# Performance work log

Hardware: AMD Instinct MI355X
Metric: run time of the kernel (lower is better)

The kernel has to match this reference:

```python
import jax, jax.numpy as jnp
import numpy as np

B, N, E, H = 16, 577, 1024, 16          # batch, tokens (1 cls + 24x24 patches), embed, heads
HD = E // H
LORA_E, LORA_R = 4, 16                   # LoRA experts, rank
AD_E, AD_D = 4, 64                       # adapter experts, bottleneck
FF = 4 * E


def setup_inputs() -> dict:
    key = jax.random.key(0)
    ks = jax.random.split(key, 12)
    p = lambda i, shape: jax.random.normal(ks[i], shape, dtype=jnp.float32) * 0.02
    return {
        "tokens": jax.random.normal(ks[0], (B, N, E), dtype=jnp.float32),
        "ln1_g": jnp.ones((E,), jnp.float32), "ln1_b": jnp.zeros((E,), jnp.float32),
        "qkv_w": p(1, (3 * E, E)), "qkv_b": jnp.zeros((3 * E,), jnp.float32),
        "proj_w": p(2, (E, E)), "proj_b": jnp.zeros((E,), jnp.float32),
        "lora_gate_w": p(3, (LORA_E, E)),
        "lora_A": p(4, (LORA_E, LORA_R, E)),
        "lora_B": p(5, (LORA_E, 3 * E, LORA_R)),
        "ln2_g": jnp.ones((E,), jnp.float32), "ln2_b": jnp.zeros((E,), jnp.float32),
        "fc1_w": p(6, (FF, E)), "fc1_b": jnp.zeros((FF,), jnp.float32),
        "fc2_w": p(7, (E, FF)), "fc2_b": jnp.zeros((E,), jnp.float32),
        "ad_gate_w": p(8, (AD_E, E)),
        "ad_down_w": p(9, (AD_E, AD_D, E)), "ad_down_b": jnp.zeros((AD_E, AD_D), jnp.float32),
        "ad_up_w": p(10, (AD_E, E, AD_D)), "ad_up_b": jnp.zeros((AD_E, E), jnp.float32),
    }


def _ln(x, g, b):
    m = x.mean(-1, keepdims=True)
    v = ((x - m) ** 2).mean(-1, keepdims=True)
    return (x - m) * jax.lax.rsqrt(v + 1e-6) * g + b


def reference(tokens, ln1_g, ln1_b, qkv_w, qkv_b, proj_w, proj_b,
              lora_gate_w, lora_A, lora_B, ln2_g, ln2_b,
              fc1_w, fc1_b, fc2_w, fc2_b,
              ad_gate_w, ad_down_w, ad_down_b, ad_up_w, ad_up_b):
    # ---- attention with MoE-LoRA delta on fused QKV ----
    normed = _ln(tokens, ln1_g, ln1_b)                      # [B,N,E]
    qkv = normed @ qkv_w.T + qkv_b                          # [B,N,3E]
    gates = jax.nn.softmax(normed @ lora_gate_w.T, axis=-1)  # [B,N,X]
    h = jnp.einsum('bnd,xrd->bnxr', normed, lora_A)         # low-rank down
    delta = jnp.einsum('bnxr,bnx,xor->bno', h, gates, lora_B)  # gate-weighted up
    qkv = (qkv + delta).reshape(B, N, 3, H, HD).transpose(2, 0, 3, 1, 4)
    q, k, v = qkv[0], qkv[1], qkv[2]                        # [B,H,N,hd]
    scores = jnp.einsum('bhqd,bhkd->bhqk', q, k) * (HD ** -0.5)
    probs = jax.nn.softmax(scores, axis=-1)
    ctx = jnp.einsum('bhqk,bhkd->bhqd', probs, v)
    ctx = ctx.transpose(0, 2, 1, 3).reshape(B, N, E)
    tokens = tokens + (ctx @ proj_w.T + proj_b)
    # ---- MLP + MoE adapter branch (shared norm2 input) ----
    mlp_in = _ln(tokens, ln2_g, ln2_b)
    mlp_out = jax.nn.gelu(mlp_in @ fc1_w.T + fc1_b, approximate=False) @ fc2_w.T + fc2_b
    ag = jax.nn.softmax(mlp_in @ ad_gate_w.T, axis=-1)       # [B,N,Xa]
    ah = jax.nn.gelu(jnp.einsum('bnd,xhd->bnxh', mlp_in, ad_down_w) + ad_down_b,
                     approximate=False)
    ad_out = (jnp.einsum('bnxh,bnx,xoh->bno', ah, ag, ad_up_w)
              + jnp.einsum('bnx,xo->bno', ag, ad_up_b))
    return tokens + mlp_out + ad_out
```

## Files before the change

### kernel.cpp

```cpp
#include <hip/hip_runtime.h>
#include <math.h>

#define TOK 9232
#define EMB 1024
#define NQKV 3072
#define FFD 4096
#define NSEQ 577

typedef __bf16 bf16x8 __attribute__((ext_vector_type(8)));
typedef float f32x4 __attribute__((ext_vector_type(4)));
typedef unsigned short ushort8 __attribute__((ext_vector_type(8)));
typedef unsigned short ushort4v __attribute__((ext_vector_type(4)));

typedef __attribute__((address_space(3))) unsigned int lds_u32_t;
typedef const __attribute__((address_space(1))) unsigned int glob_u32_t;

__device__ __forceinline__ void async16(void* lds, const void* g) {
    __builtin_amdgcn_global_load_lds((glob_u32_t*)g, (lds_u32_t*)lds, 16, 0, 0);
}

__device__ __forceinline__ unsigned short f2bf(float f) {
    unsigned int u = __builtin_bit_cast(unsigned int, f);
    u = (u + 0x7fffu + ((u >> 16) & 1u)) >> 16;
    return (unsigned short)u;
}
__device__ __forceinline__ float bf2f(unsigned short s) {
    unsigned int u = ((unsigned int)s) << 16;
    return __builtin_bit_cast(float, u);
}
__device__ __forceinline__ float gelu_exact(float x) {
    return 0.5f * x * (1.0f + erff(x * 0.70710678118654752f));
}

__global__ void k_f32_to_bf16(const float* __restrict__ in, unsigned short* __restrict__ out, int n) {
    int i = blockIdx.x * 256 + threadIdx.x;
    if (i < n) out[i] = f2bf(in[i]);
}
__global__ void k_pack_bcat(const float* __restrict__ Bw, unsigned short* __restrict__ out) {
    int i = blockIdx.x * 256 + threadIdx.x;
    if (i >= 4 * 3072 * 16) return;
    int x = i / (3072 * 16);
    int rem = i - x * (3072 * 16);
    int o = rem >> 4;
    int r = rem & 15;
    out[o * 64 + x * 16 + r] = f2bf(Bw[i]);
}
__global__ void k_pack_u(const float* __restrict__ Uw, unsigned short* __restrict__ out) {
    int i = blockIdx.x * 256 + threadIdx.x;
    if (i >= 4 * 1024 * 64) return;
    int x = i >> 16;
    int o = (i >> 6) & 1023;
    int h = i & 63;
    out[o * 256 + x * 64 + h] = f2bf(Uw[i]);
}

__global__ __launch_bounds__(256) void k_ln_gates(const float* __restrict__ x,
                                                  const float* __restrict__ g,
                                                  const float* __restrict__ b,
                                                  const float* __restrict__ gw,
                                                  unsigned short* __restrict__ out,
                                                  float* __restrict__ gates) {
    int t = blockIdx.x;
    int tid = threadIdx.x;
    const float* xp = x + (size_t)t * EMB;
    float4 v = ((const float4*)xp)[tid];
    float s = v.x + v.y + v.z + v.w;
    float sq = v.x * v.x + v.y * v.y + v.z * v.z + v.w * v.w;
    #pragma unroll
    for (int off = 32; off > 0; off >>= 1) {
        s += __shfl_down(s, off);
        sq += __shfl_down(sq, off);
    }
    __shared__ float red[8];
    if ((tid & 63) == 0) { red[tid >> 6] = s; red[(tid >> 6) + 4] = sq; }
    __syncthreads();
    float S = red[0] + red[1] + red[2] + red[3];
    float SQ = red[4] + red[5] + red[6] + red[7];
    float mean = S * (1.0f / EMB);
    float var = SQ * (1.0f / EMB) - mean * mean;
    float rstd = rsqrtf(var + 1e-6f);
    float4 gv = ((const float4*)g)[tid];
    float4 bv = ((const float4*)b)[tid];
    float n0 = (v.x - mean) * rstd * gv.x + bv.x;
    float n1 = (v.y - mean) * rstd * gv.y + bv.y;
    float n2 = (v.z - mean) * rstd * gv.z + bv.z;
    float n3 = (v.w - mean) * rstd * gv.w + bv.w;
    ushort4v o;
    o[0] = f2bf(n0); o[1] = f2bf(n1); o[2] = f2bf(n2); o[3] = f2bf(n3);
    ((ushort4v*)(out + (size_t)t * EMB))[tid] = o;
    float p[4];
    #pragma unroll
    for (int xx = 0; xx < 4; ++xx) {
        float4 gr = ((const float4*)(gw + xx * EMB))[tid];
        p[xx] = n0 * gr.x + n1 * gr.y + n2 * gr.z + n3 * gr.w;
    }
    #pragma unroll
    for (int off = 32; off > 0; off >>= 1) {
        #pragma unroll
        for (int xx = 0; xx < 4; ++xx) p[xx] += __shfl_down(p[xx], off);
    }
    __shared__ float red2[4][4];
    if ((tid & 63) == 0) {
        #pragma unroll
        for (int xx = 0; xx < 4; ++xx) red2[tid >> 6][xx] = p[xx];
    }
    __syncthreads();
    if (tid == 0) {
        float l[4];
        #pragma unroll
        for (int xx = 0; xx < 4; ++xx) l[xx] = red2[0][xx] + red2[1][xx] + red2[2][xx] + red2[3][xx];
        float m = fmaxf(fmaxf(l[0], l[1]), fmaxf(l[2], l[3]));
        float e[4], ssum = 0.f;
        #pragma unroll
        for (int xx = 0; xx < 4; ++xx) { e[xx] = expf(l[xx] - m); ssum += e[xx]; }
        float inv = 1.0f / ssum;
        #pragma unroll
        for (int xx = 0; xx < 4; ++xx) gates[t * 4 + xx] = e[xx] * inv;
    }
}

__global__ void k_make_hw(const float* __restrict__ gates, const float* __restrict__ lh,
                          unsigned short* __restrict__ hw) {
    int i = blockIdx.x * 256 + threadIdx.x;
    if (i >= TOK * 64) return;
    int t = i >> 6;
    int j = i & 63;
    hw[i] = f2bf(gates[t * 4 + (j >> 4)] * lh[i]);
}

__global__ void k_make_ahw(const float* __restrict__ ag, const float* __restrict__ ahpre,
                           unsigned short* __restrict__ ahw) {
    int i = blockIdx.x * 256 + threadIdx.x;
    if (i >= TOK * 256) return;
    int t = i >> 8;
    int j = i & 255;
    ahw[i] = f2bf(ag[t * 4 + (j >> 6)] * gelu_exact(ahpre[i]));
}

__global__ __launch_bounds__(256) void k_adbias(const float* __restrict__ ag,
                                                const float* __restrict__ upb,
                                                float* __restrict__ tok2) {
    int t = blockIdx.x;
    int tid = threadIdx.x;
    float g0 = ag[t * 4 + 0], g1 = ag[t * 4 + 1], g2 = ag[t * 4 + 2], g3 = ag[t * 4 + 3];
    float4 b0 = ((const float4*)(upb + 0 * EMB))[tid];
    float4 b1 = ((const float4*)(upb + 1 * EMB))[tid];
    float4 b2 = ((const float4*)(upb + 2 * EMB))[tid];
    float4 b3 = ((const float4*)(upb + 3 * EMB))[tid];
    float4 r = ((float4*)(tok2 + (size_t)t * EMB))[tid];
    r.x += g0 * b0.x + g1 * b1.x + g2 * b2.x + g3 * b3.x;
    r.y += g0 * b0.y + g1 * b1.y + g2 * b2.y + g3 * b3.y;
    r.z += g0 * b0.z + g1 * b1.z + g2 * b2.z + g3 * b3.z;
    r.w += g0 * b0.w + g1 * b1.w + g2 * b2.w + g3 * b3.w;
    ((float4*)(tok2 + (size_t)t * EMB))[tid] = r;
}

template<bool GELU, bool BF16OUT>
__global__ __launch_bounds__(256) void k_gemm(
    const unsigned short* __restrict__ A, const unsigned short* __restrict__ W,
    int M, int N, int K,
    const unsigned short* __restrict__ A2, const unsigned short* __restrict__ W2, int K2,
    const float* __restrict__ bias, const float* __restrict__ resid,
    void* __restrict__ Cout, int ldc, int gy)
{
    __shared__ unsigned short As[128][32];
    __shared__ unsigned short Ws[128][32];
    int tid = threadIdx.x;

    int nwg = gridDim.x;
    int orig = blockIdx.x;
    int xcd = orig & 7, lid = orig >> 3;
    int q = nwg >> 3, r = nwg & 7;
    int wg = (xcd < r ? xcd * (q + 1) : r * (q + 1) + (xcd - r) * q) + lid;
    int bm128 = (wg / gy) * 128;
    int bn128 = (wg % gy) * 128;

    int l = tid & 63, w = tid >> 6;
    int wr = w >> 1, wc = w & 1;
    int lr = l & 15, lk = (l >> 4) * 8;
    int srow = l >> 2;
    int sslot = (l & 3) * 8;

    f32x4 acc[4][4];
    #pragma unroll
    for (int m = 0; m < 4; ++m)
        #pragma unroll
        for (int n = 0; n < 4; ++n) acc[m][n] = (f32x4){0.f, 0.f, 0.f, 0.f};

    auto kloop = [&](const unsigned short* __restrict__ Ap,
                     const unsigned short* __restrict__ Wp, int Kc) {
        for (int k0 = 0; k0 < Kc; k0 += 32) {
            #pragma unroll
            for (int i = 0; i < 2; ++i) {
                int row = w * 32 + i * 16 + srow;
                int ra = bm128 + row; if (ra >= M) ra = M - 1;
                async16((char*)&As[0][0] + w * 2048 + i * 1024,
                        Ap + (size_t)ra * Kc + k0 + sslot);
                int rb = bn128 + row; if (rb >= N) rb = N - 1;
                async16((char*)&Ws[0][0] + w * 2048 + i * 1024,
                        Wp + (size_t)rb * Kc + k0 + sslot);
            }
            __syncthreads();
            bf16x8 af[4], bfr[4];
            #pragma unroll
            for (int m = 0; m < 4; ++m) af[m] = *(const bf16x8*)&As[wr * 64 + m * 16 + lr][lk];
            #pragma unroll
            for (int n = 0; n < 4; ++n) bfr[n] = *(const bf16x8*)&Ws[wc * 64 + n * 16 + lr][lk];
            #pragma unroll
            for (int m = 0; m < 4; ++m)
                #pragma unroll
                for (int n = 0; n < 4; ++n)
                    acc[m][n] = __builtin_amdgcn_mfma_f32_16x16x32_bf16(af[m], bfr[n], acc[m][n], 0, 0, 0);
            __syncthreads();
        }
    };
    kloop(A, W, K);
    if (A2) kloop(A2, W2, K2);

    int rb0 = bm128 + wr * 64;
    int cb0 = bn128 + wc * 64;
    #pragma unroll
    for (int n = 0; n < 4; ++n) {
        int col = cb0 + n * 16 + lr;
        if (col >= N) continue;
        float bv = bias ? bias[col] : 0.0f;
        #pragma unroll
        for (int m = 0; m < 4; ++m) {
            #pragma unroll
            for (int rr = 0; rr < 4; ++rr) {
                int row = rb0 + m * 16 + (l >> 4) * 4 + rr;
                if (row >= M) continue;
                float c = acc[m][n][rr] + bv;
                if (GELU) c = gelu_exact(c);
                if (resid) c += resid[(size_t)row * ldc + col];
                if (BF16OUT) ((unsigned short*)Cout)[(size_t)row * ldc + col] = f2bf(c);
                else ((float*)Cout)[(size_t)row * ldc + col] = c;
            }
        }
    }
}

__global__ __launch_bounds__(256) void k_attn(const unsigned short* __restrict__ qkv,
                                              unsigned short* __restrict__ ctx) {
    int bh = blockIdx.x;
    int qt = blockIdx.y;
    int b = bh >> 4, h = bh & 15;
    int tid = threadIdx.x;
    int l = tid & 63;
    int w = tid >> 6;
    int lr = l & 15;
    int lk = (l >> 4) * 8;

    __shared__ unsigned short Qs[64][72];
    __shared__ unsigned short Ks[64][72];
    __shared__ unsigned short Vt[64][72];
    __shared__ unsigned short Ps[64][72];

    const size_t base = (size_t)b * NSEQ * NQKV + (size_t)h * 64;
    int q0 = qt * 64;

    {
        int row = tid >> 2, ds = (tid & 3) * 16;
        int qrow = q0 + row;
        if (qrow < NSEQ) {
            const unsigned short* src = qkv + base + (size_t)qrow * NQKV + ds;
            #pragma unroll
            for (int j = 0; j < 16; ++j) Qs[row][ds + j] = f2bf(bf2f(src[j]) * 0.125f);
        } else {
            #pragma unroll
            for (int j = 0; j < 16; ++j) Qs[row][ds + j] = 0;
        }
    }

    float m_run[4], l_run[4];
    f32x4 o[4];
    #pragma unroll
    for (int r = 0; r < 4; ++r) { m_run[r] = -1e30f; l_run[r] = 0.0f; }
    #pragma unroll
    for (int n = 0; n < 4; ++n) o[n] = (f32x4){0.f, 0.f, 0.f, 0.f};

    for (int kt = 0; kt < 10; ++kt) {
        __syncthreads();
        {
            int row = tid >> 2, ds = (tid & 3) * 16;
            int key = kt * 64 + row;
            if (key < NSEQ) {
                const unsigned short* ksrc = qkv + base + (size_t)key * NQKV + 1024 + ds;
                *(ushort8*)&Ks[row][ds] = *(const ushort8*)ksrc;
                *(ushort8*)&Ks[row][ds + 8] = *(const ushort8*)(ksrc + 8);
                const unsigned short* vsrc = qkv + base + (size_t)key * NQKV + 2048 + ds;
                #pragma unroll
                for (int j = 0; j < 16; ++j) Vt[ds + j][row] = vsrc[j];
            } else {
                ushort8 z = {};
                *(ushort8*)&Ks[row][ds] = z;
                *(ushort8*)&Ks[row][ds + 8] = z;
                #pragma unroll
                for (int j = 0; j < 16; ++j) Vt[ds + j][row] = 0;
            }
        }
        __syncthreads();

        f32x4 s[4];
        #pragma unroll
        for (int n = 0; n < 4; ++n) s[n] = (f32x4){0.f, 0.f, 0.f, 0.f};
        #pragma unroll
        for (int ks = 0; ks < 2; ++ks) {
            bf16x8 qa = *(const bf16x8*)&Qs[w * 16 + lr][ks * 32 + lk];
            #pragma unroll
            for (int n = 0; n < 4; ++n) {
                bf16x8 kb = *(const bf16x8*)&Ks[n * 16 + lr][ks * 32 + lk];
                s[n] = __builtin_amdgcn_mfma_f32_16x16x32_bf16(qa, kb, s[n], 0, 0, 0);
            }
        }
        #pragma unroll
        for (int n = 0; n < 4; ++n) {
            int col = kt * 64 + n * 16 + lr;
            if (col >= NSEQ) {
                #pragma unroll
                for (int r = 0; r < 4; ++r) s[n][r] = -1e30f;
            }
        }
        float tmax[4];
        #pragma unroll
        for (int r = 0; r < 4; ++r)
            tmax[r] = fmaxf(fmaxf(s[0][r], s[1][r]), fmaxf(s[2][r], s[3][r]));
        #pragma unroll
        for (int off = 1; off < 16; off <<= 1) {
            #pragma unroll
            for (int r = 0; r < 4; ++r) tmax[r] = fmaxf(tmax[r], __shfl_xor(tmax[r], off));
        }
        float alpha[4], rs[4];
        #pragma unroll
        for (int r = 0; r < 4; ++r) {
            float mn = fmaxf(m_run[r], tmax[r]);
            alpha[r] = __expf(m_run[r] - mn);
            m_run[r] = mn;
            rs[r] = 0.0f;
        }
        #pragma unroll
        for (int n = 0; n < 4; ++n) {
            #pragma unroll
            for (int r = 0; r < 4; ++r) {
                float p = __expf(s[n][r] - m_run[r]);
                s[n][r] = p;
                rs[r] += p;
            }
        }
        #pragma unroll
        for (int off = 1; off < 16; off <<= 1) {
            #pragma unroll
            for (int r = 0; r < 4; ++r) rs[r] += __shfl_xor(rs[r], off);
        }
        #pragma unroll
        for (int r = 0; r < 4; ++r) l_run[r] = l_run[r] * alpha[r] + rs[r];
        #pragma unroll
        for (int n = 0; n < 4; ++n) {
            #pragma unroll
            for (int r = 0; r < 4; ++r) o[n][r] *= alpha[r];
        }
        #pragma unroll
        for (int n = 0; n < 4; ++n) {
            #pragma unroll
            for (int r = 0; r < 4; ++r)
                Ps[w * 16 + (l >> 4) * 4 + r][n * 16 + lr] = f2bf(s[n][r]);
        }
        __syncthreads();
        #pragma unroll
        for (int ks = 0; ks < 2; ++ks) {
            bf16x8 pa = *(const bf16x8*)&Ps[w * 16 + lr][ks * 32 + lk];
            #pragma unroll
            for (int n = 0; n < 4; ++n) {
                bf16x8 vb = *(const bf16x8*)&Vt[n * 16 + lr][ks * 32 + lk];
                o[n] = __builtin_amdgcn_mfma_f32_16x16x32_bf16(pa, vb, o[n], 0, 0, 0);
            }
        }
    }
    #pragma unroll
    for (int r = 0; r < 4; ++r) {
        int qrow = q0 + w * 16 + (l >> 4) * 4 + r;
        if (qrow < NSEQ) {
            float inv = (l_run[r] > 0.f) ? 1.0f / l_run[r] : 0.0f;
            #pragma unroll
            for (int n = 0; n < 4; ++n)
                ctx[((size_t)b * NSEQ + qrow) * EMB + h * 64 + n * 16 + lr] = f2bf(o[n][r] * inv);
        }
    }
}

extern "C" void kernel_launch(void* const* d_in, const int* in_sizes, int n_in,
                              void* d_out, int out_size, void* d_ws, size_t ws_size,
                              hipStream_t stream) {
    const float* tokens      = (const float*)d_in[0];
    const float* ln1_g       = (const float*)d_in[1];
    const float* ln1_b       = (const float*)d_in[2];
    const float* qkv_w       = (const float*)d_in[3];
    const float* qkv_b       = (const float*)d_in[4];
    const float* proj_w      = (const float*)d_in[5];
    const float* proj_b      = (const float*)d_in[6];
    const float* lora_gate_w = (const float*)d_in[7];
    const float* lora_A      = (const float*)d_in[8];
    const float* lora_B      = (const float*)d_in[9];
    const float* ln2_g       = (const float*)d_in[10];
    const float* ln2_b       = (const float*)d_in[11];
    const float* fc1_w       = (const float*)d_in[12];
    const float* fc1_b       = (const float*)d_in[13];
    const float* fc2_w       = (const float*)d_in[14];
    const float* fc2_b       = (const float*)d_in[15];
    const float* ad_gate_w   = (const float*)d_in[16];
    const float* ad_down_w   = (const float*)d_in[17];
    const float* ad_down_b   = (const float*)d_in[18];
    const float* ad_up_w     = (const float*)d_in[19];
    const float* ad_up_b     = (const float*)d_in[20];

    char* ws = (char*)d_ws;
    size_t off = 0;
    auto alloc = [&](size_t bytes) -> void* {
        void* p = ws + off;
        off += (bytes + 255) & ~(size_t)255;
        return p;
    };

    unsigned short* w_qkv  = (unsigned short*)alloc((size_t)NQKV * EMB * 2);
    unsigned short* w_proj = (unsigned short*)alloc((size_t)EMB * EMB * 2);
    unsigned short* w_fc1  = (unsigned short*)alloc((size_t)FFD * EMB * 2);
    unsigned short* w_fc2  = (unsigned short*)alloc((size_t)EMB * FFD * 2);
    unsigned short* w_acat = (unsigned short*)alloc((size_t)64 * EMB * 2);
    unsigned short* w_bcat = (unsigned short*)alloc((size_t)NQKV * 64 * 2);
    unsigned short* w_dcat = (unsigned short*)alloc((size_t)256 * EMB * 2);
    unsigned short* w_u    = (unsigned short*)alloc((size_t)EMB * 256 * 2);

    unsigned short* u1 = (unsigned short*)alloc((size_t)TOK * EMB * 2);
    char*           u2 = (char*)alloc((size_t)TOK * EMB * 2);
    unsigned short* u3 = (unsigned short*)alloc((size_t)TOK * FFD * 2);
    float* tok2   = (float*)alloc((size_t)TOK * EMB * 4);
    float* lora_h = (float*)alloc((size_t)TOK * 64 * 4);
    unsigned short* hw = (unsigned short*)alloc((size_t)TOK * 64 * 2);
    float* gates = (float*)alloc((size_t)TOK * 4 * 4);
    float* ag    = (float*)alloc((size_t)TOK * 4 * 4);

    unsigned short* normed = u1;
    unsigned short* mlpin  = u1;
    unsigned short* ctx    = (unsigned short*)u2;
    float*          ahpre  = (float*)u2;
    unsigned short* ahw    = (unsigned short*)(u2 + (size_t)TOK * 256 * 4);
    unsigned short* qkv    = u3;
    unsigned short* h1     = u3;

    k_f32_to_bf16<<<(NQKV * EMB + 255) / 256, 256, 0, stream>>>(qkv_w, w_qkv, NQKV * EMB);
    k_f32_to_bf16<<<(EMB * EMB + 255) / 256, 256, 0, stream>>>(proj_w, w_proj, EMB * EMB);
    k_f32_to_bf16<<<(FFD * EMB + 255) / 256, 256, 0, stream>>>(fc1_w, w_fc1, FFD * EMB);
    k_f32_to_bf16<<<(EMB * FFD + 255) / 256, 256, 0, stream>>>(fc2_w, w_fc2, EMB * FFD);
    k_f32_to_bf16<<<(64 * EMB + 255) / 256, 256, 0, stream>>>(lora_A, w_acat, 64 * EMB);
    k_pack_bcat<<<(NQKV * 64 + 255) / 256, 256, 0, stream>>>(lora_B, w_bcat);
    k_f32_to_bf16<<<(256 * EMB + 255) / 256, 256, 0, stream>>>(ad_down_w, w_dcat, 256 * EMB);
    k_pack_u<<<(EMB * 256 + 255) / 256, 256, 0, stream>>>(ad_up_w, w_u);

    k_ln_gates<<<TOK, 256, 0, stream>>>(tokens, ln1_g, ln1_b, lora_gate_w, normed, gates);
    k_gemm<false, false><<<73 * 1, 256, 0, stream>>>(
        normed, w_acat, TOK, 64, EMB, nullptr, nullptr, 0, nullptr, nullptr, lora_h, 64, 1);
    k_make_hw<<<(TOK * 64 + 255) / 256, 256, 0, stream>>>(gates, lora_h, hw);
    k_gemm<false, true><<<73 * 24, 256, 0, stream>>>(
        normed, w_qkv, TOK, NQKV, EMB, hw, w_bcat, 64, qkv_b, nullptr, qkv, NQKV, 24);
    k_attn<<<dim3(256, 10), 256, 0, stream>>>(qkv, ctx);
    k_gemm<false, false><<<73 * 8, 256, 0, stream>>>(
        ctx, w_proj, TOK, EMB, EMB, nullptr, nullptr, 0, proj_b, tokens, tok2, EMB, 8);
    k_ln_gates<<<TOK, 256, 0, stream>>>(tok2, ln2_g, ln2_b, ad_gate_w, mlpin, ag);
    k_gemm<false, false><<<73 * 2, 256, 0, stream>>>(
        mlpin, w_dcat, TOK, 256, EMB, nullptr, nullptr, 0, ad_down_b, nullptr, ahpre, 256, 2);
    k_make_ahw<<<(TOK * 256 + 255) / 256, 256, 0, stream>>>(ag, ahpre, ahw);
    k_adbias<<<TOK, 256, 0, stream>>>(ag, ad_up_b, tok2);
    k_gemm<true, true><<<73 * 32, 256, 0, stream>>>(
        mlpin, w_fc1, TOK, FFD, EMB, nullptr, nullptr, 0, fc1_b, nullptr, h1, FFD, 32);
    k_gemm<false, false><<<73 * 8, 256, 0, stream>>>(
        h1, w_fc2, TOK, EMB, FFD, ahw, w_u, 256, fc2_b, tok2, d_out, EMB, 8);
}
```

Measured before the change: 785.6 us.

## Fuse gating into GEMM epilogues, split-K fc2 with atomics, batch weight packing

```diff
diff --git a/kernel.cpp b/kernel.cpp
--- a/kernel.cpp
+++ b/kernel.cpp
@@ -32,26 +32,38 @@
     return 0.5f * x * (1.0f + erff(x * 0.70710678118654752f));
 }
 
-__global__ void k_f32_to_bf16(const float* __restrict__ in, unsigned short* __restrict__ out, int n) {
-    int i = blockIdx.x * 256 + threadIdx.x;
-    if (i < n) out[i] = f2bf(in[i]);
+__global__ void k_pack_all(const float* __restrict__ s_qkv, const float* __restrict__ s_proj,
+                           const float* __restrict__ s_fc1, const float* __restrict__ s_fc2,
+                           const float* __restrict__ s_la,  const float* __restrict__ s_ad,
+                           unsigned short* __restrict__ d_qkv, unsigned short* __restrict__ d_proj,
+                           unsigned short* __restrict__ d_fc1, unsigned short* __restrict__ d_fc2,
+                           unsigned short* __restrict__ d_la,  unsigned short* __restrict__ d_ad) {
+    int stride = gridDim.x * 256;
+    for (int i4 = blockIdx.x * 256 + threadIdx.x; i4 < 3227648; i4 += stride) {
+        const float* s; unsigned short* d; int local;
+        if (i4 < 786432)       { s = s_qkv;  d = d_qkv;  local = i4; }
+        else if (i4 < 1048576) { s = s_proj; d = d_proj; local = i4 - 786432; }
+        else if (i4 < 2097152) { s = s_fc1;  d = d_fc1;  local = i4 - 1048576; }
+        else if (i4 < 3145728) { s = s_fc2;  d = d_fc2;  local = i4 - 2097152; }
+        else if (i4 < 3162112) { s = s_la;   d = d_la;   local = i4 - 3145728; }
+        else                   { s = s_ad;   d = d_ad;   local = i4 - 3162112; }
+        float4 v = ((const float4*)s)[local];
+        ushort4v o;
+        o[0] = f2bf(v.x); o[1] = f2bf(v.y); o[2] = f2bf(v.z); o[3] = f2bf(v.w);
+        ((ushort4v*)d)[local] = o;
+    }
 }
 __global__ void k_pack_bcat(const float* __restrict__ Bw, unsigned short* __restrict__ out) {
     int i = blockIdx.x * 256 + threadIdx.x;
-    if (i >= 4 * 3072 * 16) return;
-    int x = i / (3072 * 16);
-    int rem = i - x * (3072 * 16);
-    int o = rem >> 4;
-    int r = rem & 15;
-    out[o * 64 + x * 16 + r] = f2bf(Bw[i]);
+    if (i >= 3072 * 64) return;
+    int o = i >> 6, j = i & 63, x = j >> 4, r = j & 15;
+    out[o * 64 + j] = f2bf(Bw[x * 3072 * 16 + o * 16 + r]);
 }
 __global__ void k_pack_u(const float* __restrict__ Uw, unsigned short* __restrict__ out) {
     int i = blockIdx.x * 256 + threadIdx.x;
-    if (i >= 4 * 1024 * 64) return;
-    int x = i >> 16;
-    int o = (i >> 6) & 1023;
-    int h = i & 63;
-    out[o * 256 + x * 64 + h] = f2bf(Uw[i]);
+    if (i >= 1024 * 256) return;
+    int o = i >> 8, j = i & 255, x = j >> 6, h = j & 63;
+    out[o * 256 + j] = f2bf(Uw[x * 65536 + o * 64 + h]);
 }
 
 __global__ __launch_bounds__(256) void k_ln_gates(const float* __restrict__ x,
@@ -119,27 +131,11 @@
     }
 }
 
-__global__ void k_make_hw(const float* __restrict__ gates, const float* __restrict__ lh,
-                          unsigned short* __restrict__ hw) {
-    int i = blockIdx.x * 256 + threadIdx.x;
-    if (i >= TOK * 64) return;
-    int t = i >> 6;
-    int j = i & 63;
-    hw[i] = f2bf(gates[t * 4 + (j >> 4)] * lh[i]);
-}
-
-__global__ void k_make_ahw(const float* __restrict__ ag, const float* __restrict__ ahpre,
-                           unsigned short* __restrict__ ahw) {
-    int i = blockIdx.x * 256 + threadIdx.x;
-    if (i >= TOK * 256) return;
-    int t = i >> 8;
-    int j = i & 255;
-    ahw[i] = f2bf(ag[t * 4 + (j >> 6)] * gelu_exact(ahpre[i]));
-}
-
-__global__ __launch_bounds__(256) void k_adbias(const float* __restrict__ ag,
-                                                const float* __restrict__ upb,
-                                                float* __restrict__ tok2) {
+__global__ __launch_bounds__(256) void k_fc2init(const float* __restrict__ tok2,
+                                                 const float* __restrict__ fc2b,
+                                                 const float* __restrict__ ag,
+                                                 const float* __restrict__ upb,
+                                                 float* __restrict__ out) {
     int t = blockIdx.x;
     int tid = threadIdx.x;
     float g0 = ag[t * 4 + 0], g1 = ag[t * 4 + 1], g2 = ag[t * 4 + 2], g3 = ag[t * 4 + 3];
@@ -147,33 +143,37 @@
     float4 b1 = ((const float4*)(upb + 1 * EMB))[tid];
     float4 b2 = ((const float4*)(upb + 2 * EMB))[tid];
     float4 b3 = ((const float4*)(upb + 3 * EMB))[tid];
-    float4 r = ((float4*)(tok2 + (size_t)t * EMB))[tid];
-    r.x += g0 * b0.x + g1 * b1.x + g2 * b2.x + g3 * b3.x;
-    r.y += g0 * b0.y + g1 * b1.y + g2 * b2.y + g3 * b3.y;
-    r.z += g0 * b0.z + g1 * b1.z + g2 * b2.z + g3 * b3.z;
-    r.w += g0 * b0.w + g1 * b1.w + g2 * b2.w + g3 * b3.w;
-    ((float4*)(tok2 + (size_t)t * EMB))[tid] = r;
-}
-
-template<bool GELU, bool BF16OUT>
+    float4 fb = ((const float4*)fc2b)[tid];
+    float4 r = ((const float4*)(tok2 + (size_t)t * EMB))[tid];
+    r.x += fb.x + g0 * b0.x + g1 * b1.x + g2 * b2.x + g3 * b3.x;
+    r.y += fb.y + g0 * b0.y + g1 * b1.y + g2 * b2.y + g3 * b3.y;
+    r.z += fb.z + g0 * b0.z + g1 * b1.z + g2 * b2.z + g3 * b3.z;
+    r.w += fb.w + g0 * b0.w + g1 * b1.w + g2 * b2.w + g3 * b3.w;
+    ((float4*)(out + (size_t)t * EMB))[tid] = r;
+}
+
+template<bool GELU, bool BF16OUT, bool ATOMIC, int GG, int KS>
 __global__ __launch_bounds__(256) void k_gemm(
-    const unsigned short* __restrict__ A, const unsigned short* __restrict__ W,
-    int M, int N, int K,
+    const unsigned short* __restrict__ A, int lda,
+    const unsigned short* __restrict__ W, int ldw, int klen,
+    int M, int N,
     const unsigned short* __restrict__ A2, const unsigned short* __restrict__ W2, int K2,
     const float* __restrict__ bias, const float* __restrict__ resid,
+    const float* __restrict__ aux,
     void* __restrict__ Cout, int ldc, int gy)
 {
     __shared__ unsigned short As[128][32];
     __shared__ unsigned short Ws[128][32];
     int tid = threadIdx.x;
-
-    int nwg = gridDim.x;
-    int orig = blockIdx.x;
+    int nwg = gridDim.x, orig = blockIdx.x;
     int xcd = orig & 7, lid = orig >> 3;
     int q = nwg >> 3, r = nwg & 7;
     int wg = (xcd < r ? xcd * (q + 1) : r * (q + 1) + (xcd - r) * q) + lid;
-    int bm128 = (wg / gy) * 128;
-    int bn128 = (wg % gy) * 128;
+    int mt = wg / gy, nk = wg - mt * gy;
+    int nt = nk / KS, ks = nk - nt * KS;
+    int bm128 = mt * 128;
+    int bn128 = nt * 128;
+    int koff = ks * klen;
 
     int l = tid & 63, w = tid >> 6;
     int wr = w >> 1, wc = w & 1;
@@ -187,18 +187,18 @@
         #pragma unroll
         for (int n = 0; n < 4; ++n) acc[m][n] = (f32x4){0.f, 0.f, 0.f, 0.f};
 
-    auto kloop = [&](const unsigned short* __restrict__ Ap,
-                     const unsigned short* __restrict__ Wp, int Kc) {
+    auto kloop = [&](const unsigned short* __restrict__ Ap, int sA,
+                     const unsigned short* __restrict__ Wp, int sW, int Kc) {
         for (int k0 = 0; k0 < Kc; k0 += 32) {
             #pragma unroll
             for (int i = 0; i < 2; ++i) {
                 int row = w * 32 + i * 16 + srow;
                 int ra = bm128 + row; if (ra >= M) ra = M - 1;
                 async16((char*)&As[0][0] + w * 2048 + i * 1024,
-                        Ap + (size_t)ra * Kc + k0 + sslot);
+                        Ap + (size_t)ra * sA + k0 + sslot);
                 int rb = bn128 + row; if (rb >= N) rb = N - 1;
                 async16((char*)&Ws[0][0] + w * 2048 + i * 1024,
-                        Wp + (size_t)rb * Kc + k0 + sslot);
+                        Wp + (size_t)rb * sW + k0 + sslot);
             }
             __syncthreads();
             bf16x8 af[4], bfr[4];
@@ -214,8 +214,8 @@
             __syncthreads();
         }
     };
-    kloop(A, W, K);
-    if (A2) kloop(A2, W2, K2);
+    kloop(A + koff, lda, W + koff, ldw, klen);
+    if (A2 && ks == KS - 1) kloop(A2, K2, W2, K2, K2);
 
     int rb0 = bm128 + wr * 64;
     int cb0 = bn128 + wc * 64;
@@ -232,9 +232,15 @@
                 if (row >= M) continue;
                 float c = acc[m][n][rr] + bv;
                 if (GELU) c = gelu_exact(c);
+                if (GG > 0) c *= aux[row * 4 + col / (GG > 0 ? GG : 1)];
                 if (resid) c += resid[(size_t)row * ldc + col];
-                if (BF16OUT) ((unsigned short*)Cout)[(size_t)row * ldc + col] = f2bf(c);
-                else ((float*)Cout)[(size_t)row * ldc + col] = c;
+                if (ATOMIC) {
+                    unsafeAtomicAdd((float*)Cout + (size_t)row * ldc + col, c);
+                } else if (BF16OUT) {
+                    ((unsigned short*)Cout)[(size_t)row * ldc + col] = f2bf(c);
+                } else {
+                    ((float*)Cout)[(size_t)row * ldc + col] = c;
+                }
             }
         }
     }
@@ -431,47 +437,45 @@
     unsigned short* w_u    = (unsigned short*)alloc((size_t)EMB * 256 * 2);
 
     unsigned short* u1 = (unsigned short*)alloc((size_t)TOK * EMB * 2);
-    char*           u2 = (char*)alloc((size_t)TOK * EMB * 2);
+    unsigned short* u2 = (unsigned short*)alloc((size_t)TOK * EMB * 2);
     unsigned short* u3 = (unsigned short*)alloc((size_t)TOK * FFD * 2);
-    float* tok2   = (float*)alloc((size_t)TOK * EMB * 4);
-    float* lora_h = (float*)alloc((size_t)TOK * 64 * 4);
-    unsigned short* hw = (unsigned short*)alloc((size_t)TOK * 64 * 2);
+    float* tok2  = (float*)alloc((size_t)TOK * EMB * 4);
+    unsigned short* hw  = (unsigned short*)alloc((size_t)TOK * 64 * 2);
+    unsigned short* ahw = (unsigned short*)alloc((size_t)TOK * 256 * 2);
     float* gates = (float*)alloc((size_t)TOK * 4 * 4);
     float* ag    = (float*)alloc((size_t)TOK * 4 * 4);
 
     unsigned short* normed = u1;
     unsigned short* mlpin  = u1;
-    unsigned short* ctx    = (unsigned short*)u2;
-    float*          ahpre  = (float*)u2;
-    unsigned short* ahw    = (unsigned short*)(u2 + (size_t)TOK * 256 * 4);
+    unsigned short* ctx    = u2;
     unsigned short* qkv    = u3;
     unsigned short* h1     = u3;
 
-    k_f32_to_bf16<<<(NQKV * EMB + 255) / 256, 256, 0, stream>>>(qkv_w, w_qkv, NQKV * EMB);
-    k_f32_to_bf16<<<(EMB * EMB + 255) / 256, 256, 0, stream>>>(proj_w, w_proj, EMB * EMB);
-    k_f32_to_bf16<<<(FFD * EMB + 255) / 256, 256, 0, stream>>>(fc1_w, w_fc1, FFD * EMB);
-    k_f32_to_bf16<<<(EMB * FFD + 255) / 256, 256, 0, stream>>>(fc2_w, w_fc2, EMB * FFD);
-    k_f32_to_bf16<<<(64 * EMB + 255) / 256, 256, 0, stream>>>(lora_A, w_acat, 64 * EMB);
+    k_pack_all<<<2048, 256, 0, stream>>>(qkv_w, proj_w, fc1_w, fc2_w, lora_A, ad_down_w,
+                                         w_qkv, w_proj, w_fc1, w_fc2, w_acat, w_dcat);
     k_pack_bcat<<<(NQKV * 64 + 255) / 256, 256, 0, stream>>>(lora_B, w_bcat);
-    k_f32_to_bf16<<<(256 * EMB + 255) / 256, 256, 0, stream>>>(ad_down_w, w_dcat, 256 * EMB);
     k_pack_u<<<(EMB * 256 + 255) / 256, 256, 0, stream>>>(ad_up_w, w_u);
 
     k_ln_gates<<<TOK, 256, 0, stream>>>(tokens, ln1_g, ln1_b, lora_gate_w, normed, gates);
-    k_gemm<false, false><<<73 * 1, 256, 0, stream>>>(
-        normed, w_acat, TOK, 64, EMB, nullptr, nullptr, 0, nullptr, nullptr, lora_h, 64, 1);
-    k_make_hw<<<(TOK * 64 + 255) / 256, 256, 0, stream>>>(gates, lora_h, hw);
-    k_gemm<false, true><<<73 * 24, 256, 0, stream>>>(
-        normed, w_qkv, TOK, NQKV, EMB, hw, w_bcat, 64, qkv_b, nullptr, qkv, NQKV, 24);
+    k_gemm<false, true, false, 16, 1><<<73, 256, 0, stream>>>(
+        normed, EMB, w_acat, EMB, EMB, TOK, 64,
+        nullptr, nullptr, 0, nullptr, nullptr, gates, hw, 64, 1);
+    k_gemm<false, true, false, 0, 1><<<73 * 24, 256, 0, stream>>>(
+        normed, EMB, w_qkv, EMB, EMB, TOK, NQKV,
+        hw, w_bcat, 64, qkv_b, nullptr, nullptr, qkv, NQKV, 24);
     k_attn<<<dim3(256, 10), 256, 0, stream>>>(qkv, ctx);
-    k_gemm<false, false><<<73 * 8, 256, 0, stream>>>(
-        ctx, w_proj, TOK, EMB, EMB, nullptr, nullptr, 0, proj_b, tokens, tok2, EMB, 8);
+    k_gemm<false, false, false, 0, 1><<<73 * 8, 256, 0, stream>>>(
+        ctx, EMB, w_proj, EMB, EMB, TOK, EMB,
+        nullptr, nullptr, 0, proj_b, tokens, nullptr, tok2, EMB, 8);
     k_ln_gates<<<TOK, 256, 0, stream>>>(tok2, ln2_g, ln2_b, ad_gate_w, mlpin, ag);
-    k_gemm<false, false><<<73 * 2, 256, 0, stream>>>(
-        mlpin, w_dcat, TOK, 256, EMB, nullptr, nullptr, 0, ad_down_b, nullptr, ahpre, 256, 2);
-    k_make_ahw<<<(TOK * 256 + 255) / 256, 256, 0, stream>>>(ag, ahpre, ahw);
-    k_adbias<<<TOK, 256, 0, stream>>>(ag, ad_up_b, tok2);
-    k_gemm<true, true><<<73 * 32, 256, 0, stream>>>(
-        mlpin, w_fc1, TOK, FFD, EMB, nullptr, nullptr, 0, fc1_b, nullptr, h1, FFD, 32);
-    k_gemm<false, false><<<73 * 8, 256, 0, stream>>>(
-        h1, w_fc2, TOK, EMB, FFD, ahw, w_u, 256, fc2_b, tok2, d_out, EMB, 8);
-}
+    k_gemm<true, true, false, 64, 1><<<73 * 2, 256, 0, stream>>>(
+        mlpin, EMB, w_dcat, EMB, EMB, TOK, 256,
+        nullptr, nullptr, 0, ad_down_b, nullptr, ag, ahw, 256, 2);
+    k_fc2init<<<TOK, 256, 0, stream>>>(tok2, fc2_b, ag, ad_up_b, (float*)d_out);
+    k_gemm<true, true, false, 0, 1><<<73 * 32, 256, 0, stream>>>(
+        mlpin, EMB, w_fc1, EMB, EMB, TOK, FFD,
+        nullptr, nullptr, 0, fc1_b, nullptr, nullptr, h1, FFD, 32);
+    k_gemm<false, false, true, 0, 2><<<73 * 16, 256, 0, stream>>>(
+        h1, FFD, w_fc2, FFD, 2048, TOK, EMB,
+        ahw, w_u, 256, nullptr, nullptr, nullptr, (float*)d_out, EMB, 16);
+}
```

Result: slower. 806.4 us (+2.6%).
